# Kernel optimization log

Measured on AMD Instinct MI355X. Metric: run time of the kernel, lower is better.

The kernel has to match this reference:

```python
import jax, jax.numpy as jnp
import numpy as np

H, W = 1024, 2048      # dims from __init__
C = 34                 # Cityscapes label ids 0..33 (thing classes 24..33)
N_INST = 128           # instance capacity (len(instance_probs))


def setup_inputs() -> dict:
    key = jax.random.key(0)
    k1, k2, k3, k4 = jax.random.split(key, 4)
    return {
        "segmentation_map": jax.random.randint(k1, (H, W), 0, C, dtype=jnp.int32),
        "instance_maps": jax.random.randint(k2, (H, W), 0, N_INST + 1, dtype=jnp.int32),
        "seg_map_probs": jax.random.uniform(k3, (C, H, W), dtype=jnp.float32),
        "instance_probs": jax.random.uniform(k4, (N_INST,), dtype=jnp.float32),
    }


def reference(segmentation_map, instance_maps, seg_map_probs, instance_probs):
    # nn.Threshold(23.99, 50): x if x > 23.99 else 50; then things = (thresh <= 33)
    seg_f = segmentation_map.astype(jnp.float32)
    things = (seg_f > 23.99) & (seg_f <= 33.0)           # (H, W) bool
    inst = jnp.where(things, instance_maps, 0)            # zero-out non-thing pixels

    flat_inst = inst.reshape(-1)                          # (HW,)
    flat_seg = segmentation_map.reshape(-1)               # (HW,)

    # segmented histogram: pixel counts per (instance, class)
    pair_idx = flat_inst * C + flat_seg
    counts2d = jax.ops.segment_sum(
        jnp.ones_like(flat_inst), pair_idx, num_segments=(N_INST + 1) * C
    ).reshape(N_INST + 1, C)

    # segmented sum of every class prob map over each instance mask
    probs_pix = seg_map_probs.reshape(C, -1).T            # (HW, C)
    sums2d = jax.ops.segment_sum(probs_pix, flat_inst, num_segments=N_INST + 1)  # (N+1, C)

    counts = counts2d[1:]                                 # drop background id 0 -> (N, C)
    sums = sums2d[1:]                                     # (N, C)

    inst_class = jnp.argmax(counts, axis=1).astype(jnp.int32)     # mode class per instance
    total = counts.sum(axis=1)                                     # seg_counts.sum()
    # mean of the winning class's prob map over the instance mask
    seg_prob = jnp.take_along_axis(sums, inst_class[:, None], axis=1)[:, 0] / jnp.maximum(
        total, 1
    ).astype(seg_map_probs.dtype)

    # per-instance binary masks, uint8 like the torch code
    inst_ids = jnp.arange(1, N_INST + 1, dtype=inst.dtype)
    inst_masks = (inst[None, :, :] == inst_ids[:, None, None]).astype(jnp.uint8)  # (N, H, W)

    valid = total > 0   # which instance slots actually appear in the image
    return inst_masks, inst_class, instance_probs, seg_prob, total, valid
```

## Files before the change

### kernel.cpp

```cpp
#include <hip/hip_runtime.h>

#define HH   1024
#define WW   2048
#define HWP  (HH * WW)
#define CC   34
#define NI   128
#define THING_LO 24
#define THING_HI 33
#define NTC  10

typedef float nfloat4 __attribute__((ext_vector_type(4)));

#define OFF_CLASS  ((size_t)NI * HWP)
#define OFF_PROBS  (OFF_CLASS + NI)
#define OFF_SEGP   (OFF_PROBS + NI)
#define OFF_TOTAL  (OFF_SEGP + NI)
#define OFF_VALID  (OFF_TOTAL + NI)

#define WS_COUNTS  0
#define WS_SEGSUM  (NI * NTC * 4)
#define WS_CLS     (WS_SEGSUM + NI * 4)
#define WS_TOT     (WS_CLS + NI * 4)

__device__ __forceinline__ int thing_inst(int s, int im) {
    return (s >= THING_LO && s <= THING_HI) ? im : 0;
}

__global__ __launch_bounds__(256) void k1_mask_count(
    const int* __restrict__ seg, const int* __restrict__ imap,
    float* __restrict__ out_masks, int* __restrict__ counts)
{
    const int t = blockIdx.x * 256 + threadIdx.x;
    const int p = t * 4;
    const int4 sg = *reinterpret_cast<const int4*>(seg + p);
    const int4 im = *reinterpret_cast<const int4*>(imap + p);

    const int i0 = thing_inst(sg.x, im.x);
    const int i1 = thing_inst(sg.y, im.y);
    const int i2 = thing_inst(sg.z, im.z);
    const int i3 = thing_inst(sg.w, im.w);

    if (i0 > 0) atomicAdd(&counts[(i0 - 1) * NTC + (sg.x - THING_LO)], 1);
    if (i1 > 0) atomicAdd(&counts[(i1 - 1) * NTC + (sg.y - THING_LO)], 1);
    if (i2 > 0) atomicAdd(&counts[(i2 - 1) * NTC + (sg.z - THING_LO)], 1);
    if (i3 > 0) atomicAdd(&counts[(i3 - 1) * NTC + (sg.w - THING_LO)], 1);

    float* o = out_masks + p;
    #pragma unroll
    for (int i = 1; i <= NI; ++i) {
        nfloat4 v;
        v.x = (i0 == i) ? 1.0f : 0.0f;
        v.y = (i1 == i) ? 1.0f : 0.0f;
        v.z = (i2 == i) ? 1.0f : 0.0f;
        v.w = (i3 == i) ? 1.0f : 0.0f;
        __builtin_nontemporal_store(v, reinterpret_cast<nfloat4*>(o));
        o += HWP;
    }
}

__global__ __launch_bounds__(128) void k2_stats(
    const int* __restrict__ counts, const float* __restrict__ iprobs,
    float* __restrict__ out, int* __restrict__ cls_ws,
    int* __restrict__ tot_ws, float* __restrict__ seg_sum)
{
    const int i = threadIdx.x;
    int bestv = 0, bestc = 0, tot = 0;
    #pragma unroll
    for (int j = 0; j < NTC; ++j) {
        const int c = counts[i * NTC + j];
        tot += c;
        if (c > bestv) { bestv = c; bestc = THING_LO + j; }
    }
    cls_ws[i] = bestc;
    tot_ws[i] = tot;
    seg_sum[i] = 0.0f;
    out[OFF_CLASS + i] = (float)bestc;
    out[OFF_PROBS + i] = iprobs[i];
    out[OFF_TOTAL + i] = (float)tot;
    out[OFF_VALID + i] = (tot > 0) ? 1.0f : 0.0f;
}

__global__ __launch_bounds__(256) void k3_segsum(
    const int* __restrict__ seg, const int* __restrict__ imap,
    const float* __restrict__ probs, const int* __restrict__ cls_ws,
    float* __restrict__ seg_sum)
{
    __shared__ float lsum[NI];
    __shared__ int   scls[NI];
    if (threadIdx.x < NI) {
        lsum[threadIdx.x] = 0.0f;
        scls[threadIdx.x] = cls_ws[threadIdx.x];
    }
    __syncthreads();

    const int stride = gridDim.x * blockDim.x;
    for (int t = blockIdx.x * blockDim.x + threadIdx.x; t < HWP / 4; t += stride) {
        const int p = t * 4;
        const int4 sg = *reinterpret_cast<const int4*>(seg + p);
        const int4 im = *reinterpret_cast<const int4*>(imap + p);
        const int ii[4] = { thing_inst(sg.x, im.x), thing_inst(sg.y, im.y),
                            thing_inst(sg.z, im.z), thing_inst(sg.w, im.w) };
        #pragma unroll
        for (int k = 0; k < 4; ++k) {
            if (ii[k] > 0) {
                const int inst = ii[k] - 1;
                const size_t idx = (size_t)scls[inst] * HWP + (size_t)(p + k);
                atomicAdd(&lsum[inst], probs[idx]);
            }
        }
    }
    __syncthreads();
    if (threadIdx.x < NI) {
        const float v = lsum[threadIdx.x];
        if (v != 0.0f) atomicAdd(&seg_sum[threadIdx.x], v);
    }
}

__global__ __launch_bounds__(128) void k4_segprob(
    const float* __restrict__ seg_sum, const int* __restrict__ tot_ws,
    float* __restrict__ out)
{
    const int i = threadIdx.x;
    const int t = tot_ws[i];
    out[OFF_SEGP + i] = seg_sum[i] / (float)(t > 0 ? t : 1);
}

extern "C" void kernel_launch(void* const* d_in, const int* in_sizes, int n_in,
                              void* d_out, int out_size, void* d_ws, size_t ws_size,
                              hipStream_t stream) {
    const int*   seg    = (const int*)d_in[0];
    const int*   imap   = (const int*)d_in[1];
    const float* probs  = (const float*)d_in[2];
    const float* iprobs = (const float*)d_in[3];
    float* out = (float*)d_out;

    char* ws = (char*)d_ws;
    int*   counts  = (int*)(ws + WS_COUNTS);
    float* seg_sum = (float*)(ws + WS_SEGSUM);
    int*   cls_ws  = (int*)(ws + WS_CLS);
    int*   tot_ws  = (int*)(ws + WS_TOT);

    (void)hipMemsetAsync(counts, 0, NI * NTC * sizeof(int), stream);

    const int grid1 = (HWP / 4) / 256;
    k1_mask_count<<<grid1, 256, 0, stream>>>(seg, imap, out, counts);
    k2_stats<<<1, 128, 0, stream>>>(counts, iprobs, out, cls_ws, tot_ws, seg_sum);
    k3_segsum<<<256, 256, 0, stream>>>(seg, imap, probs, cls_ws, seg_sum);
    k4_segprob<<<1, 128, 0, stream>>>(seg_sum, tot_ws, out);
}
```

Measured before the change: 1.286 ms.

## Pack instance ids into bytes and split mask writing into plane-chunked kernel

A prep kernel now builds a byte-packed instance-id map (4 pixels per word) and the pixel-class histogram in one pass. A separate kernel then writes the 128 mask planes, each block covering one plane chunk and re-reading the small packed map instead of the two full int32 inputs. The segment-sum kernel reads the packed map too, uses one thread per 16 pixels over a full grid, and folds the final division into its atomic add on the output, which removes the last kernel. The cost is an extra workspace buffer and repeated reads of the packed map for every plane, which should mostly hit in cache.

```diff
diff --git a/kernel.cpp b/kernel.cpp
--- a/kernel.cpp
+++ b/kernel.cpp
@@ -18,17 +18,17 @@
 #define OFF_VALID  (OFF_TOTAL + NI)
 
 #define WS_COUNTS  0
-#define WS_SEGSUM  (NI * NTC * 4)
-#define WS_CLS     (WS_SEGSUM + NI * 4)
-#define WS_TOT     (WS_CLS + NI * 4)
+#define WS_CLS     (NI * NTC * 4)
+#define WS_INV     (WS_CLS + NI * 4)
+#define WS_INST    8192
 
 __device__ __forceinline__ int thing_inst(int s, int im) {
     return (s >= THING_LO && s <= THING_HI) ? im : 0;
 }
 
-__global__ __launch_bounds__(256) void k1_mask_count(
+__global__ __launch_bounds__(256) void k0_prep(
     const int* __restrict__ seg, const int* __restrict__ imap,
-    float* __restrict__ out_masks, int* __restrict__ counts)
+    unsigned int* __restrict__ inst_pack, int* __restrict__ counts)
 {
     const int t = blockIdx.x * 256 + threadIdx.x;
     const int p = t * 4;
@@ -40,28 +40,18 @@
     const int i2 = thing_inst(sg.z, im.z);
     const int i3 = thing_inst(sg.w, im.w);
 
+    inst_pack[t] = (unsigned)i0 | ((unsigned)i1 << 8) |
+                   ((unsigned)i2 << 16) | ((unsigned)i3 << 24);
+
     if (i0 > 0) atomicAdd(&counts[(i0 - 1) * NTC + (sg.x - THING_LO)], 1);
     if (i1 > 0) atomicAdd(&counts[(i1 - 1) * NTC + (sg.y - THING_LO)], 1);
     if (i2 > 0) atomicAdd(&counts[(i2 - 1) * NTC + (sg.z - THING_LO)], 1);
     if (i3 > 0) atomicAdd(&counts[(i3 - 1) * NTC + (sg.w - THING_LO)], 1);
-
-    float* o = out_masks + p;
-    #pragma unroll
-    for (int i = 1; i <= NI; ++i) {
-        nfloat4 v;
-        v.x = (i0 == i) ? 1.0f : 0.0f;
-        v.y = (i1 == i) ? 1.0f : 0.0f;
-        v.z = (i2 == i) ? 1.0f : 0.0f;
-        v.w = (i3 == i) ? 1.0f : 0.0f;
-        __builtin_nontemporal_store(v, reinterpret_cast<nfloat4*>(o));
-        o += HWP;
-    }
 }
 
 __global__ __launch_bounds__(128) void k2_stats(
     const int* __restrict__ counts, const float* __restrict__ iprobs,
-    float* __restrict__ out, int* __restrict__ cls_ws,
-    int* __restrict__ tot_ws, float* __restrict__ seg_sum)
+    float* __restrict__ out, int* __restrict__ cls_ws, float* __restrict__ inv_ws)
 {
     const int i = threadIdx.x;
     int bestv = 0, bestc = 0, tot = 0;
@@ -72,18 +62,43 @@
         if (c > bestv) { bestv = c; bestc = THING_LO + j; }
     }
     cls_ws[i] = bestc;
-    tot_ws[i] = tot;
-    seg_sum[i] = 0.0f;
+    inv_ws[i] = 1.0f / (float)(tot > 0 ? tot : 1);
     out[OFF_CLASS + i] = (float)bestc;
     out[OFF_PROBS + i] = iprobs[i];
+    out[OFF_SEGP  + i] = 0.0f;
     out[OFF_TOTAL + i] = (float)tot;
     out[OFF_VALID + i] = (tot > 0) ? 1.0f : 0.0f;
 }
 
+#define MCHUNK_PX 32768
+#define MCHUNKS   (HWP / MCHUNK_PX)
+__global__ __launch_bounds__(256) void k_mask(
+    const unsigned int* __restrict__ inst_pack, float* __restrict__ out)
+{
+    const int plane = blockIdx.x >> 6;
+    const int chunk = blockIdx.x & 63;
+    const unsigned pid = (unsigned)(plane + 1);
+    const size_t base_px = (size_t)chunk * MCHUNK_PX;
+    float* oplane = out + (size_t)plane * HWP + base_px;
+    const unsigned int* ip = inst_pack + (base_px >> 2);
+
+    #pragma unroll 8
+    for (int j = 0; j < MCHUNK_PX / (256 * 4); ++j) {
+        const int q = j * 256 + threadIdx.x;
+        const unsigned int w = ip[q];
+        nfloat4 v;
+        v.x = ((w & 255u)         == pid) ? 1.0f : 0.0f;
+        v.y = (((w >> 8) & 255u)  == pid) ? 1.0f : 0.0f;
+        v.z = (((w >> 16) & 255u) == pid) ? 1.0f : 0.0f;
+        v.w = ((w >> 24)          == pid) ? 1.0f : 0.0f;
+        __builtin_nontemporal_store(v, reinterpret_cast<nfloat4*>(oplane + q * 4));
+    }
+}
+
 __global__ __launch_bounds__(256) void k3_segsum(
-    const int* __restrict__ seg, const int* __restrict__ imap,
-    const float* __restrict__ probs, const int* __restrict__ cls_ws,
-    float* __restrict__ seg_sum)
+    const unsigned int* __restrict__ inst_pack, const float* __restrict__ probs,
+    const int* __restrict__ cls_ws, const float* __restrict__ inv_ws,
+    float* __restrict__ out)
 {
     __shared__ float lsum[NI];
     __shared__ int   scls[NI];
@@ -93,36 +108,29 @@
     }
     __syncthreads();
 
-    const int stride = gridDim.x * blockDim.x;
-    for (int t = blockIdx.x * blockDim.x + threadIdx.x; t < HWP / 4; t += stride) {
-        const int p = t * 4;
-        const int4 sg = *reinterpret_cast<const int4*>(seg + p);
-        const int4 im = *reinterpret_cast<const int4*>(imap + p);
-        const int ii[4] = { thing_inst(sg.x, im.x), thing_inst(sg.y, im.y),
-                            thing_inst(sg.z, im.z), thing_inst(sg.w, im.w) };
+    const int t = blockIdx.x * 256 + threadIdx.x;
+    const uint4 wv = reinterpret_cast<const uint4*>(inst_pack)[t];
+    const int base_px = t * 16;
+    const unsigned wvs[4] = { wv.x, wv.y, wv.z, wv.w };
+    #pragma unroll
+    for (int wi = 0; wi < 4; ++wi) {
+        const unsigned w = wvs[wi];
         #pragma unroll
         for (int k = 0; k < 4; ++k) {
-            if (ii[k] > 0) {
-                const int inst = ii[k] - 1;
-                const size_t idx = (size_t)scls[inst] * HWP + (size_t)(p + k);
-                atomicAdd(&lsum[inst], probs[idx]);
+            const int inst = (int)((w >> (8 * k)) & 255u);
+            if (inst > 0) {
+                const size_t idx = (size_t)scls[inst - 1] * HWP +
+                                   (size_t)(base_px + wi * 4 + k);
+                atomicAdd(&lsum[inst - 1], probs[idx]);
             }
         }
     }
     __syncthreads();
     if (threadIdx.x < NI) {
         const float v = lsum[threadIdx.x];
-        if (v != 0.0f) atomicAdd(&seg_sum[threadIdx.x], v);
+        if (v != 0.0f)
+            atomicAdd(&out[OFF_SEGP + threadIdx.x], v * inv_ws[threadIdx.x]);
     }
-}
-
-__global__ __launch_bounds__(128) void k4_segprob(
-    const float* __restrict__ seg_sum, const int* __restrict__ tot_ws,
-    float* __restrict__ out)
-{
-    const int i = threadIdx.x;
-    const int t = tot_ws[i];
-    out[OFF_SEGP + i] = seg_sum[i] / (float)(t > 0 ? t : 1);
 }
 
 extern "C" void kernel_launch(void* const* d_in, const int* in_sizes, int n_in,
@@ -135,16 +143,15 @@
     float* out = (float*)d_out;
 
     char* ws = (char*)d_ws;
-    int*   counts  = (int*)(ws + WS_COUNTS);
-    float* seg_sum = (float*)(ws + WS_SEGSUM);
-    int*   cls_ws  = (int*)(ws + WS_CLS);
-    int*   tot_ws  = (int*)(ws + WS_TOT);
+    int*          counts    = (int*)(ws + WS_COUNTS);
+    int*          cls_ws    = (int*)(ws + WS_CLS);
+    float*        inv_ws    = (float*)(ws + WS_INV);
+    unsigned int* inst_pack = (unsigned int*)(ws + WS_INST);
 
     (void)hipMemsetAsync(counts, 0, NI * NTC * sizeof(int), stream);
 
-    const int grid1 = (HWP / 4) / 256;
-    k1_mask_count<<<grid1, 256, 0, stream>>>(seg, imap, out, counts);
-    k2_stats<<<1, 128, 0, stream>>>(counts, iprobs, out, cls_ws, tot_ws, seg_sum);
-    k3_segsum<<<256, 256, 0, stream>>>(seg, imap, probs, cls_ws, seg_sum);
-    k4_segprob<<<1, 128, 0, stream>>>(seg_sum, tot_ws, out);
+    k0_prep<<<(HWP / 4) / 256, 256, 0, stream>>>(seg, imap, inst_pack, counts);
+    k2_stats<<<1, 128, 0, stream>>>(counts, iprobs, out, cls_ws, inv_ws);
+    k_mask<<<NI * MCHUNKS, 256, 0, stream>>>(inst_pack, out);
+    k3_segsum<<<(HWP / 16) / 256, 256, 0, stream>>>(inst_pack, probs, cls_ws, inv_ws, out);
 }
```

Measured after the change: 1.336 ms. 3.9% more time.
